# Kernel tuning notes

Measured on AMD Instinct MI355X. Metric: run time of the kernel, lower is better.

The kernel has to match this reference:

```python
import jax, jax.numpy as jnp
import numpy as np

EMBED, H1, H2, IMG, MID, VOCAB = 1024, 1024, 1024, 2048, 512, 32000
N_REGIONS = 576


def lstm_cell(x, h, c, W_ih, W_hh, b_ih, b_hh):
    # PyTorch LSTM gate order: i, f, g, o
    g = x @ W_ih.T + b_ih + h @ W_hh.T + b_hh
    i, f, gg, o = jnp.split(g, 4, axis=-1)
    i, f, o = jax.nn.sigmoid(i), jax.nn.sigmoid(f), jax.nn.sigmoid(o)
    c_new = f * c + i * jnp.tanh(gg)
    h_new = o * jnp.tanh(c_new)
    return h_new, c_new


def setup_inputs() -> dict:
    key = jax.random.key(0)
    ks = jax.random.split(key, 24)
    s = 0.02
    in1 = H2 + IMG + EMBED   # lstm1 input size = 4096
    in2 = H1 + IMG           # lstm2 input size = 3072
    return {
        "V": jax.random.normal(ks[0], (N_REGIONS, IMG), jnp.float32),
        "w": jax.random.randint(ks[1], (1,), 0, VOCAB),
        "h1": jax.random.normal(ks[2], (1, 1, H1), jnp.float32),
        "c1": jax.random.normal(ks[3], (1, 1, H1), jnp.float32),
        "h2": jax.random.normal(ks[4], (1, 1, H2), jnp.float32),
        "c2": jax.random.normal(ks[5], (1, 1, H2), jnp.float32),
        "emb": jax.random.normal(ks[6], (VOCAB, EMBED), jnp.float32) * s,
        "W_ih1": jax.random.normal(ks[7], (4 * H1, in1), jnp.float32) * s,
        "W_hh1": jax.random.normal(ks[8], (4 * H1, H1), jnp.float32) * s,
        "b_ih1": jax.random.normal(ks[9], (4 * H1,), jnp.float32) * s,
        "b_hh1": jax.random.normal(ks[10], (4 * H1,), jnp.float32) * s,
        "W_ih2": jax.random.normal(ks[11], (4 * H2, in2), jnp.float32) * s,
        "W_hh2": jax.random.normal(ks[12], (4 * H2, H2), jnp.float32) * s,
        "b_ih2": jax.random.normal(ks[13], (4 * H2,), jnp.float32) * s,
        "b_hh2": jax.random.normal(ks[14], (4 * H2,), jnp.float32) * s,
        "lv_w": jax.random.normal(ks[15], (MID, IMG), jnp.float32) * s,
        "lv_b": jax.random.normal(ks[16], (MID,), jnp.float32) * s,
        "lh_w": jax.random.normal(ks[17], (MID, H1), jnp.float32) * s,
        "lh_b": jax.random.normal(ks[18], (MID,), jnp.float32) * s,
        "att_w": jax.random.normal(ks[19], (1, MID), jnp.float32) * s,
        "att_b": jax.random.normal(ks[20], (1,), jnp.float32) * s,
        "lin_w": jax.random.normal(ks[21], (VOCAB, H2), jnp.float32) * s,
        "lin_b": jax.random.normal(ks[22], (VOCAB,), jnp.float32) * s,
    }


def reference(V, w, h1, c1, h2, c2, emb, W_ih1, W_hh1, b_ih1, b_hh1,
              W_ih2, W_hh2, b_ih2, b_hh2, lv_w, lv_b, lh_w, lh_b,
              att_w, att_b, lin_w, lin_b):
    vbar = V.mean(axis=0, keepdims=True)                 # [1, IMG]
    we = emb[w]                                          # [1, EMBED]
    x1 = jnp.concatenate([h2[0], vbar, we], axis=1)      # [1, H2+IMG+EMBED]
    h1n, c1n = lstm_cell(x1, h1[0], c1[0], W_ih1, W_hh1, b_ih1, b_hh1)

    vt = V @ lv_w.T + lv_b                               # [N, MID]
    h1t = h1n @ lh_w.T + lh_b                            # [1, MID] (broadcast = repeat)
    a = jnp.tanh(vt + h1t) @ att_w.T + att_b             # [N, 1]
    a = jax.nn.softmax(a, axis=0)                        # softmax over regions
    v = (a * V).sum(axis=0, keepdims=True)               # [1, IMG]

    x2 = jnp.concatenate([v, h1n], axis=1)               # [1, H1+IMG]
    h2n, c2n = lstm_cell(x2, h2[0], c2[0], W_ih2, W_hh2, b_ih2, b_hh2)

    o = h2n @ lin_w.T + lin_b                            # [1, VOCAB]
    return (o, h1n[None], c1n[None], h2n[None], c2n[None])
```

## Files before the change

kernel.cpp:

```cpp
#include <hip/hip_runtime.h>

#define H     1024
#define IMG   2048
#define MID   512
#define VOCAB 32000
#define NR    576
#define IN1   4096
#define IN2   3072
#define VN    (NR * IMG)
#define WN    (MID * IMG)

typedef unsigned short u16;
typedef unsigned int u32;
typedef __attribute__((ext_vector_type(8))) short short8;
typedef __attribute__((ext_vector_type(4))) float f32x4;

__device__ __forceinline__ float wave_sum(float v) {
  #pragma unroll
  for (int off = 32; off > 0; off >>= 1) v += __shfl_down(v, off, 64);
  return v;
}
__device__ __forceinline__ float sigf(float x) { return 1.0f / (1.0f + __expf(-x)); }
__device__ __forceinline__ float dot4(float4 a, float4 b) {
  return a.x * b.x + a.y * b.y + a.z * b.z + a.w * b.w;
}
__device__ __forceinline__ u32 f2bfbits(float f) {
  union { float f; u32 i; } c; c.f = f;
  return (c.i + 0x7fffu + ((c.i >> 16) & 1u)) >> 16;
}

__global__ __launch_bounds__(256) void k_prep(const float* __restrict__ V,
                                              const float* __restrict__ lvw,
                                              const float* __restrict__ h2,
                                              const float* __restrict__ emb,
                                              const int* __restrict__ w,
                                              u16* __restrict__ Vbf, u16* __restrict__ Wbf,
                                              float* __restrict__ x1) {
  int b = blockIdx.x;
  int t = threadIdx.x;
  if (b < 1088) {
    long i8 = (long)(b * 256 + t) * 8;
    const float* src; u16* dst; long off;
    if (i8 < VN) { src = V; dst = Vbf; off = i8; }
    else         { src = lvw; dst = Wbf; off = i8 - VN; }
    float4 qa = *(const float4*)(src + off);
    float4 qb = *(const float4*)(src + off + 4);
    u32 p0 = f2bfbits(qa.x) | (f2bfbits(qa.y) << 16);
    u32 p1 = f2bfbits(qa.z) | (f2bfbits(qa.w) << 16);
    u32 p2 = f2bfbits(qb.x) | (f2bfbits(qb.y) << 16);
    u32 p3 = f2bfbits(qb.z) | (f2bfbits(qb.w) << 16);
    *(uint4*)(dst + off) = make_uint4(p0, p1, p2, p3);
  } else if (b < 1096) {
    int tt = (b - 1088) * 256 + t;
    if (tt < H) x1[tt] = h2[tt];
    else {
      int j = tt - H;
      x1[3072 + j] = emb[(long)w[0] * 1024 + j];
    }
  } else {
    __shared__ float red[8][32];
    int bb = b - 1096;
    int c = bb * 32 + (t & 31);
    int rc = t >> 5;
    float s = 0.f;
    for (int r = rc * 72; r < rc * 72 + 72; r++) s += V[(long)r * IMG + c];
    red[rc][t & 31] = s;
    __syncthreads();
    if (t < 32) {
      float tot = 0.f;
      #pragma unroll
      for (int j = 0; j < 8; j++) tot += red[j][t];
      x1[H + bb * 32 + t] = tot * (1.0f / 576.0f);
    }
  }
}

__global__ __launch_bounds__(256) void k_gemm_lstm1(const u16* __restrict__ Vbf,
                                                    const u16* __restrict__ Wbf,
                                                    float* __restrict__ vtp,
                                                    const float* __restrict__ Wih,
                                                    const float* __restrict__ Whh,
                                                    const float* __restrict__ bih,
                                                    const float* __restrict__ bhh,
                                                    const float* __restrict__ x1,
                                                    const float* __restrict__ h1,
                                                    const float* __restrict__ c1,
                                                    float* __restrict__ h1n,
                                                    float* __restrict__ out_h,
                                                    float* __restrict__ out_c) {
  int t = threadIdx.x;
  int b = blockIdx.x;
  if (b < 288) {
    int z = b / 72, rem = b % 72;
    int bx = rem % 9, by = rem / 9;
    int wave = t >> 6, lane = t & 63;
    int wm = wave >> 1, wn = wave & 1;
    int m0 = bx * 64 + wm * 32;
    int n0 = by * 64 + wn * 32;
    int ri = lane & 15, quad = lane >> 4;
    const u16* aptr0 = Vbf + (long)(m0 + ri) * IMG + z * 512 + quad * 8;
    const u16* aptr1 = aptr0 + 16 * IMG;
    const u16* bptr0 = Wbf + (long)(n0 + ri) * IMG + z * 512 + quad * 8;
    const u16* bptr1 = bptr0 + 16 * IMG;
    f32x4 acc00 = {0.f,0.f,0.f,0.f}, acc01 = {0.f,0.f,0.f,0.f};
    f32x4 acc10 = {0.f,0.f,0.f,0.f}, acc11 = {0.f,0.f,0.f,0.f};
    #pragma unroll 4
    for (int ks = 0; ks < 16; ks++) {
      int ko = ks * 32;
      short8 a0 = *(const short8*)(aptr0 + ko);
      short8 a1 = *(const short8*)(aptr1 + ko);
      short8 b0 = *(const short8*)(bptr0 + ko);
      short8 b1 = *(const short8*)(bptr1 + ko);
      acc00 = __builtin_amdgcn_mfma_f32_16x16x32_bf16(a0, b0, acc00, 0, 0, 0);
      acc01 = __builtin_amdgcn_mfma_f32_16x16x32_bf16(a0, b1, acc01, 0, 0, 0);
      acc10 = __builtin_amdgcn_mfma_f32_16x16x32_bf16(a1, b0, acc10, 0, 0, 0);
      acc11 = __builtin_amdgcn_mfma_f32_16x16x32_bf16(a1, b1, acc11, 0, 0, 0);
    }
    float* base = vtp + (long)z * (NR * MID);
    #pragma unroll
    for (int r = 0; r < 4; r++) {
      int row = quad * 4 + r;
      base[(long)(m0 + row) * MID + n0 + ri]           = acc00[r];
      base[(long)(m0 + row) * MID + n0 + 16 + ri]      = acc01[r];
      base[(long)(m0 + 16 + row) * MID + n0 + ri]      = acc10[r];
      base[(long)(m0 + 16 + row) * MID + n0 + 16 + ri] = acc11[r];
    }
  } else {
    __shared__ float gate[4];
    int w = t >> 6, l = t & 63;
    int k = b - 288;
    int row = k + w * H;
    const float4* W4  = (const float4*)(Wih + (long)row * IN1);
    const float4* Wh4 = (const float4*)(Whh + (long)row * H);
    const float4* X4  = (const float4*)x1;
    const float4* H14 = (const float4*)h1;
    float acc = 0.f;
    #pragma unroll
    for (int c = 0; c < 16; c++) { int idx = c * 64 + l; acc += dot4(W4[idx], X4[idx]); }
    #pragma unroll
    for (int c = 0; c < 4; c++)  { int idx = c * 64 + l; acc += dot4(Wh4[idx], H14[idx]); }
    acc = wave_sum(acc);
    if (l == 0) gate[w] = acc + bih[row] + bhh[row];
    __syncthreads();
    if (t == 0) {
      float i  = sigf(gate[0]);
      float f  = sigf(gate[1]);
      float gg = tanhf(gate[2]);
      float o  = sigf(gate[3]);
      float c  = f * c1[k] + i * gg;
      float h  = o * tanhf(c);
      h1n[k] = h; out_h[k] = h; out_c[k] = c;
    }
  }
}

__global__ void k_h1t(const float* __restrict__ lhw, const float* __restrict__ lhb,
                      const float* __restrict__ h1n, float* __restrict__ h1t) {
  int w = threadIdx.x >> 6, l = threadIdx.x & 63;
  int row = blockIdx.x * 4 + w;
  const float4* W4 = (const float4*)(lhw + (long)row * H);
  const float4* X4 = (const float4*)h1n;
  float acc = 0.f;
  #pragma unroll
  for (int c = 0; c < 4; c++) { int idx = c * 64 + l; acc += dot4(W4[idx], X4[idx]); }
  acc = wave_sum(acc);
  if (l == 0) h1t[row] = acc + lhb[row];
}

__global__ void k_att(const float* __restrict__ vtp, const float* __restrict__ lvb,
                      const float* __restrict__ h1t,
                      const float* __restrict__ attw, const float* __restrict__ attb,
                      float* __restrict__ logits) {
  int w = threadIdx.x >> 6, l = threadIdx.x & 63;
  int row = blockIdx.x * 4 + w;
  const float4* A4 = (const float4*)attw;
  const float4* T4 = (const float4*)h1t;
  const float4* B4 = (const float4*)lvb;
  float acc = 0.f;
  #pragma unroll
  for (int ch = 0; ch < 2; ch++) {
    int idx = 2 * l + ch;
    const float4* p = (const float4*)(vtp + (long)row * MID) + idx;
    float4 s = p[0];
    float4 s1 = p[NR * MID / 4];
    float4 s2 = p[2 * NR * MID / 4];
    float4 s3 = p[3 * NR * MID / 4];
    float4 bb = B4[idx], tt = T4[idx], aa = A4[idx];
    float vx = s.x + s1.x + s2.x + s3.x + bb.x + tt.x;
    float vy = s.y + s1.y + s2.y + s3.y + bb.y + tt.y;
    float vz = s.z + s1.z + s2.z + s3.z + bb.z + tt.z;
    float vw = s.w + s1.w + s2.w + s3.w + bb.w + tt.w;
    acc += tanhf(vx) * aa.x + tanhf(vy) * aa.y + tanhf(vz) * aa.z + tanhf(vw) * aa.w;
  }
  acc = wave_sum(acc);
  if (l == 0) logits[row] = acc + attb[0];
}

__global__ __launch_bounds__(256) void k_smwv(const float* __restrict__ logits,
                                              const float* __restrict__ V,
                                              float* __restrict__ v) {
  __shared__ float arr[576];
  __shared__ float r8[8];
  __shared__ float red[8][32];
  int t = threadIdx.x;
  int wv = t >> 6, l = t & 63;
  float x0 = logits[t];
  float x1 = logits[t + 256];
  float x2 = (t < 64) ? logits[t + 512] : -3.0e38f;
  float m = fmaxf(fmaxf(x0, x1), x2);
  #pragma unroll
  for (int off = 32; off > 0; off >>= 1) m = fmaxf(m, __shfl_down(m, off, 64));
  if (l == 0) r8[wv] = m;
  __syncthreads();
  float bm = fmaxf(fmaxf(r8[0], r8[1]), fmaxf(r8[2], r8[3]));
  float e0 = __expf(x0 - bm);
  float e1 = __expf(x1 - bm);
  float e2 = (t < 64) ? __expf(x2 - bm) : 0.f;
  arr[t] = e0; arr[t + 256] = e1;
  if (t < 64) arr[t + 512] = e2;
  float s = wave_sum(e0 + e1 + e2);
  if (l == 0) r8[4 + wv] = s;
  __syncthreads();
  float inv = 1.0f / (r8[4] + r8[5] + r8[6] + r8[7]);
  int c = blockIdx.x * 32 + (t & 31);
  int rc = t >> 5;
  float acc = 0.f;
  #pragma unroll 8
  for (int r = rc * 72; r < rc * 72 + 72; r++) acc += arr[r] * V[(long)r * IMG + c];
  red[rc][t & 31] = acc;
  __syncthreads();
  if (t < 32) {
    float tot = 0.f;
    #pragma unroll
    for (int j = 0; j < 8; j++) tot += red[j][t];
    v[blockIdx.x * 32 + t] = tot * inv;
  }
}

__global__ __launch_bounds__(256) void k_lstm2(const float* __restrict__ Wih,
                                               const float* __restrict__ Whh,
                                               const float* __restrict__ bih,
                                               const float* __restrict__ bhh,
                                               const float* __restrict__ v,
                                               const float* __restrict__ h1n,
                                               const float* __restrict__ h2,
                                               const float* __restrict__ c2,
                                               float* __restrict__ h2n,
                                               float* __restrict__ out_h,
                                               float* __restrict__ out_c) {
  __shared__ float gate[4];
  int w = threadIdx.x >> 6, l = threadIdx.x & 63;
  int k = blockIdx.x;
  int row = k + w * H;
  const float4* W4  = (const float4*)(Wih + (long)row * IN2);
  const float4* Wh4 = (const float4*)(Whh + (long)row * H);
  const float4* Vv4 = (const float4*)v;
  const float4* H1n = (const float4*)h1n;
  const float4* H24 = (const float4*)h2;
  float acc = 0.f;
  #pragma unroll
  for (int c = 0; c < 8; c++) { int idx = c * 64 + l; acc += dot4(W4[idx], Vv4[idx]); }
  #pragma unroll
  for (int c = 0; c < 4; c++) { int idx = c * 64 + l; acc += dot4(W4[512 + idx], H1n[idx]); }
  #pragma unroll
  for (int c = 0; c < 4; c++) { int idx = c * 64 + l; acc += dot4(Wh4[idx], H24[idx]); }
  acc = wave_sum(acc);
  if (l == 0) gate[w] = acc + bih[row] + bhh[row];
  __syncthreads();
  if (threadIdx.x == 0) {
    float i  = sigf(gate[0]);
    float f  = sigf(gate[1]);
    float gg = tanhf(gate[2]);
    float o  = sigf(gate[3]);
    float c  = f * c2[k] + i * gg;
    float h  = o * tanhf(c);
    h2n[k] = h; out_h[k] = h; out_c[k] = c;
  }
}

__global__ void k_out(const float* __restrict__ linw, const float* __restrict__ linb,
                      const float* __restrict__ h2n, float* __restrict__ o) {
  int w = threadIdx.x >> 6, l = threadIdx.x & 63;
  int row = blockIdx.x * 4 + w;
  const float4* W4 = (const float4*)(linw + (long)row * H);
  const float4* X4 = (const float4*)h2n;
  float acc = 0.f;
  #pragma unroll
  for (int c = 0; c < 4; c++) { int idx = c * 64 + l; acc += dot4(W4[idx], X4[idx]); }
  acc = wave_sum(acc);
  if (l == 0) o[row] = acc + linb[row];
}

extern "C" void kernel_launch(void* const* d_in, const int* in_sizes, int n_in,
                              void* d_out, int out_size, void* d_ws, size_t ws_size,
                              hipStream_t stream) {
  const float* V    = (const float*)d_in[0];
  const int*   w    = (const int*)d_in[1];
  const float* h1   = (const float*)d_in[2];
  const float* c1   = (const float*)d_in[3];
  const float* h2   = (const float*)d_in[4];
  const float* c2   = (const float*)d_in[5];
  const float* emb  = (const float*)d_in[6];
  const float* Wih1 = (const float*)d_in[7];
  const float* Whh1 = (const float*)d_in[8];
  const float* bih1 = (const float*)d_in[9];
  const float* bhh1 = (const float*)d_in[10];
  const float* Wih2 = (const float*)d_in[11];
  const float* Whh2 = (const float*)d_in[12];
  const float* bih2 = (const float*)d_in[13];
  const float* bhh2 = (const float*)d_in[14];
  const float* lvw  = (const float*)d_in[15];
  const float* lvb  = (const float*)d_in[16];
  const float* lhw  = (const float*)d_in[17];
  const float* lhb  = (const float*)d_in[18];
  const float* attw = (const float*)d_in[19];
  const float* attb = (const float*)d_in[20];
  const float* linw = (const float*)d_in[21];
  const float* linb = (const float*)d_in[22];

  float* ws     = (float*)d_ws;
  float* x1     = ws;
  float* h1n    = ws + 4096;
  float* h1t    = ws + 5120;
  float* logits = ws + 5632;
  float* v      = ws + 6272;
  float* h2n    = ws + 8320;
  float* vtp    = ws + 9344;
  u16*   Vbf    = (u16*)(ws + 1188992);
  u16*   Wbf    = Vbf + VN;

  float* out    = (float*)d_out;
  float* out_o  = out;
  float* out_h1 = out + VOCAB;
  float* out_c1 = out + VOCAB + H;
  float* out_h2 = out + VOCAB + 2 * H;
  float* out_c2 = out + VOCAB + 3 * H;

  k_prep<<<1160, 256, 0, stream>>>(V, lvw, h2, emb, w, Vbf, Wbf, x1);
  k_gemm_lstm1<<<1312, 256, 0, stream>>>(Vbf, Wbf, vtp, Wih1, Whh1, bih1, bhh1,
                                         x1, h1, c1, h1n, out_h1, out_c1);
  k_h1t<<<128, 256, 0, stream>>>(lhw, lhb, h1n, h1t);
  k_att<<<144, 256, 0, stream>>>(vtp, lvb, h1t, attw, attb, logits);
  k_smwv<<<64, 256, 0, stream>>>(logits, V, v);
  k_lstm2<<<1024, 256, 0, stream>>>(Wih2, Whh2, bih2, bhh2, v, h1n, h2, c2, h2n, out_h2, out_c2);
  k_out<<<8000, 256, 0, stream>>>(linw, linb, h2n, out_o);
}
```

Baseline: 401.5 us.

## Drop split-K in V GEMM and hoist LSTM2 h-dependent partials into h1t kernel

The V×lv_w GEMM moves from 4-way split-K (288 blocks writing four partial slabs) to 72 blocks that each cover the full K range. The attention kernel therefore reads a single vtp slab instead of summing four. LSTM2's h1n and h2 contributions, plus its biases, are now computed early in the same launch as h1t, so the final LSTM2 kernel only does the v·W_ih2 part. The aim is to shorten the critical path after the softmax and cut vtp memory traffic. The cost is far fewer GEMM blocks, each with a longer serial K loop, which lowers parallelism in that phase.

```diff
diff --git a/kernel.cpp b/kernel.cpp
--- a/kernel.cpp
+++ b/kernel.cpp
@@ -90,22 +90,21 @@
                                                     float* __restrict__ out_c) {
   int t = threadIdx.x;
   int b = blockIdx.x;
-  if (b < 288) {
-    int z = b / 72, rem = b % 72;
-    int bx = rem % 9, by = rem / 9;
+  if (b < 72) {
+    int bx = b % 9, by = b / 9;
     int wave = t >> 6, lane = t & 63;
     int wm = wave >> 1, wn = wave & 1;
     int m0 = bx * 64 + wm * 32;
     int n0 = by * 64 + wn * 32;
     int ri = lane & 15, quad = lane >> 4;
-    const u16* aptr0 = Vbf + (long)(m0 + ri) * IMG + z * 512 + quad * 8;
+    const u16* aptr0 = Vbf + (long)(m0 + ri) * IMG + quad * 8;
     const u16* aptr1 = aptr0 + 16 * IMG;
-    const u16* bptr0 = Wbf + (long)(n0 + ri) * IMG + z * 512 + quad * 8;
+    const u16* bptr0 = Wbf + (long)(n0 + ri) * IMG + quad * 8;
     const u16* bptr1 = bptr0 + 16 * IMG;
     f32x4 acc00 = {0.f,0.f,0.f,0.f}, acc01 = {0.f,0.f,0.f,0.f};
     f32x4 acc10 = {0.f,0.f,0.f,0.f}, acc11 = {0.f,0.f,0.f,0.f};
     #pragma unroll 4
-    for (int ks = 0; ks < 16; ks++) {
+    for (int ks = 0; ks < 64; ks++) {
       int ko = ks * 32;
       short8 a0 = *(const short8*)(aptr0 + ko);
       short8 a1 = *(const short8*)(aptr1 + ko);
@@ -116,19 +115,18 @@
       acc10 = __builtin_amdgcn_mfma_f32_16x16x32_bf16(a1, b0, acc10, 0, 0, 0);
       acc11 = __builtin_amdgcn_mfma_f32_16x16x32_bf16(a1, b1, acc11, 0, 0, 0);
     }
-    float* base = vtp + (long)z * (NR * MID);
     #pragma unroll
     for (int r = 0; r < 4; r++) {
       int row = quad * 4 + r;
-      base[(long)(m0 + row) * MID + n0 + ri]           = acc00[r];
-      base[(long)(m0 + row) * MID + n0 + 16 + ri]      = acc01[r];
-      base[(long)(m0 + 16 + row) * MID + n0 + ri]      = acc10[r];
-      base[(long)(m0 + 16 + row) * MID + n0 + 16 + ri] = acc11[r];
+      vtp[(long)(m0 + row) * MID + n0 + ri]           = acc00[r];
+      vtp[(long)(m0 + row) * MID + n0 + 16 + ri]      = acc01[r];
+      vtp[(long)(m0 + 16 + row) * MID + n0 + ri]      = acc10[r];
+      vtp[(long)(m0 + 16 + row) * MID + n0 + 16 + ri] = acc11[r];
     }
   } else {
     __shared__ float gate[4];
     int w = t >> 6, l = t & 63;
-    int k = b - 288;
+    int k = b - 72;
     int row = k + w * H;
     const float4* W4  = (const float4*)(Wih + (long)row * IN1);
     const float4* Wh4 = (const float4*)(Whh + (long)row * H);
@@ -154,17 +152,42 @@
   }
 }
 
-__global__ void k_h1t(const float* __restrict__ lhw, const float* __restrict__ lhb,
-                      const float* __restrict__ h1n, float* __restrict__ h1t) {
+__global__ __launch_bounds__(256) void k_h1t_p2(const float* __restrict__ lhw,
+                                                const float* __restrict__ lhb,
+                                                const float* __restrict__ h1n,
+                                                float* __restrict__ h1t,
+                                                const float* __restrict__ Wih2,
+                                                const float* __restrict__ Whh2,
+                                                const float* __restrict__ bih2,
+                                                const float* __restrict__ bhh2,
+                                                const float* __restrict__ h2,
+                                                float* __restrict__ part2) {
   int w = threadIdx.x >> 6, l = threadIdx.x & 63;
-  int row = blockIdx.x * 4 + w;
-  const float4* W4 = (const float4*)(lhw + (long)row * H);
-  const float4* X4 = (const float4*)h1n;
-  float acc = 0.f;
-  #pragma unroll
-  for (int c = 0; c < 4; c++) { int idx = c * 64 + l; acc += dot4(W4[idx], X4[idx]); }
-  acc = wave_sum(acc);
-  if (l == 0) h1t[row] = acc + lhb[row];
+  int b = blockIdx.x;
+  if (b < 128) {
+    int row = b * 4 + w;
+    const float4* W4 = (const float4*)(lhw + (long)row * H);
+    const float4* X4 = (const float4*)h1n;
+    float acc = 0.f;
+    #pragma unroll
+    for (int c = 0; c < 4; c++) { int idx = c * 64 + l; acc += dot4(W4[idx], X4[idx]); }
+    acc = wave_sum(acc);
+    if (l == 0) h1t[row] = acc + lhb[row];
+  } else {
+    int k = b - 128;
+    int row = k + w * H;
+    const float4* W4  = (const float4*)(Wih2 + (long)row * IN2);
+    const float4* Wh4 = (const float4*)(Whh2 + (long)row * H);
+    const float4* H1n = (const float4*)h1n;
+    const float4* H24 = (const float4*)h2;
+    float acc = 0.f;
+    #pragma unroll
+    for (int c = 0; c < 4; c++) { int idx = c * 64 + l; acc += dot4(W4[512 + idx], H1n[idx]); }
+    #pragma unroll
+    for (int c = 0; c < 4; c++) { int idx = c * 64 + l; acc += dot4(Wh4[idx], H24[idx]); }
+    acc = wave_sum(acc);
+    if (l == 0) part2[row] = acc + bih2[row] + bhh2[row];
+  }
 }
 
 __global__ void k_att(const float* __restrict__ vtp, const float* __restrict__ lvb,
@@ -176,21 +199,17 @@
   const float4* A4 = (const float4*)attw;
   const float4* T4 = (const float4*)h1t;
   const float4* B4 = (const float4*)lvb;
+  const float4* S4 = (const float4*)(vtp + (long)row * MID);
   float acc = 0.f;
   #pragma unroll
   for (int ch = 0; ch < 2; ch++) {
     int idx = 2 * l + ch;
-    const float4* p = (const float4*)(vtp + (long)row * MID) + idx;
-    float4 s = p[0];
-    float4 s1 = p[NR * MID / 4];
-    float4 s2 = p[2 * NR * MID / 4];
-    float4 s3 = p[3 * NR * MID / 4];
+    float4 s = S4[idx];
     float4 bb = B4[idx], tt = T4[idx], aa = A4[idx];
-    float vx = s.x + s1.x + s2.x + s3.x + bb.x + tt.x;
-    float vy = s.y + s1.y + s2.y + s3.y + bb.y + tt.y;
-    float vz = s.z + s1.z + s2.z + s3.z + bb.z + tt.z;
-    float vw = s.w + s1.w + s2.w + s3.w + bb.w + tt.w;
-    acc += tanhf(vx) * aa.x + tanhf(vy) * aa.y + tanhf(vz) * aa.z + tanhf(vw) * aa.w;
+    acc += tanhf(s.x + bb.x + tt.x) * aa.x
+         + tanhf(s.y + bb.y + tt.y) * aa.y
+         + tanhf(s.z + bb.z + tt.z) * aa.z
+         + tanhf(s.w + bb.w + tt.w) * aa.w;
   }
   acc = wave_sum(acc);
   if (l == 0) logits[row] = acc + attb[0];
@@ -237,35 +256,24 @@
   }
 }
 
-__global__ __launch_bounds__(256) void k_lstm2(const float* __restrict__ Wih,
-                                               const float* __restrict__ Whh,
-                                               const float* __restrict__ bih,
-                                               const float* __restrict__ bhh,
-                                               const float* __restrict__ v,
-                                               const float* __restrict__ h1n,
-                                               const float* __restrict__ h2,
-                                               const float* __restrict__ c2,
-                                               float* __restrict__ h2n,
-                                               float* __restrict__ out_h,
-                                               float* __restrict__ out_c) {
+__global__ __launch_bounds__(256) void k_lstm2f(const float* __restrict__ Wih2,
+                                                const float* __restrict__ v,
+                                                const float* __restrict__ part2,
+                                                const float* __restrict__ c2,
+                                                float* __restrict__ h2n,
+                                                float* __restrict__ out_h,
+                                                float* __restrict__ out_c) {
   __shared__ float gate[4];
   int w = threadIdx.x >> 6, l = threadIdx.x & 63;
   int k = blockIdx.x;
   int row = k + w * H;
-  const float4* W4  = (const float4*)(Wih + (long)row * IN2);
-  const float4* Wh4 = (const float4*)(Whh + (long)row * H);
+  const float4* W4  = (const float4*)(Wih2 + (long)row * IN2);
   const float4* Vv4 = (const float4*)v;
-  const float4* H1n = (const float4*)h1n;
-  const float4* H24 = (const float4*)h2;
   float acc = 0.f;
   #pragma unroll
   for (int c = 0; c < 8; c++) { int idx = c * 64 + l; acc += dot4(W4[idx], Vv4[idx]); }
-  #pragma unroll
-  for (int c = 0; c < 4; c++) { int idx = c * 64 + l; acc += dot4(W4[512 + idx], H1n[idx]); }
-  #pragma unroll
-  for (int c = 0; c < 4; c++) { int idx = c * 64 + l; acc += dot4(Wh4[idx], H24[idx]); }
   acc = wave_sum(acc);
-  if (l == 0) gate[w] = acc + bih[row] + bhh[row];
+  if (l == 0) gate[w] = acc + part2[row];
   __syncthreads();
   if (threadIdx.x == 0) {
     float i  = sigf(gate[0]);
@@ -326,6 +334,7 @@
   float* v      = ws + 6272;
   float* h2n    = ws + 8320;
   float* vtp    = ws + 9344;
+  float* part2  = ws + 9344 + 294912;
   u16*   Vbf    = (u16*)(ws + 1188992);
   u16*   Wbf    = Vbf + VN;
 
@@ -337,11 +346,11 @@
   float* out_c2 = out + VOCAB + 3 * H;
 
   k_prep<<<1160, 256, 0, stream>>>(V, lvw, h2, emb, w, Vbf, Wbf, x1);
-  k_gemm_lstm1<<<1312, 256, 0, stream>>>(Vbf, Wbf, vtp, Wih1, Whh1, bih1, bhh1,
+  k_gemm_lstm1<<<1096, 256, 0, stream>>>(Vbf, Wbf, vtp, Wih1, Whh1, bih1, bhh1,
                                          x1, h1, c1, h1n, out_h1, out_c1);
-  k_h1t<<<128, 256, 0, stream>>>(lhw, lhb, h1n, h1t);
+  k_h1t_p2<<<1152, 256, 0, stream>>>(lhw, lhb, h1n, h1t, Wih2, Whh2, bih2, bhh2, h2, part2);
   k_att<<<144, 256, 0, stream>>>(vtp, lvb, h1t, attw, attb, logits);
   k_smwv<<<64, 256, 0, stream>>>(logits, V, v);
-  k_lstm2<<<1024, 256, 0, stream>>>(Wih2, Whh2, bih2, bhh2, v, h1n, h2, c2, h2n, out_h2, out_c2);
+  k_lstm2f<<<1024, 256, 0, stream>>>(Wih2, v, part2, c2, h2n, out_h2, out_c2);
   k_out<<<8000, 256, 0, stream>>>(linw, linb, h2n, out_o);
 }
```

Measured after the change: 430.4 us. 7.2% more time.
